# Optimization experiments

Hardware: AMD Instinct MI355X
Metric: run time of the kernel (lower is better)

The kernel has to match this reference:

```python
import jax, jax.numpy as jnp
import numpy as np

B, L, D, H, DH = 1, 256, 128, 4, 32  # batch, seq, d_pair, n_head, d_hidden


def setup_inputs() -> dict:
    key = jax.random.key(0)
    ks = jax.random.split(key, 8)
    s = 0.02  # init scale for weights
    return {
        "pair": jax.random.normal(ks[0], (B, L, L, D), jnp.float32),
        "ln_w": jnp.ones((D,), jnp.float32),
        "ln_b": jnp.zeros((D,), jnp.float32),
        "Wq": jax.random.normal(ks[1], (D, H * DH), jnp.float32) * s,
        "Wk": jax.random.normal(ks[2], (D, H * DH), jnp.float32) * s,
        "Wv": jax.random.normal(ks[3], (D, H * DH), jnp.float32) * s,
        "Wb": jax.random.normal(ks[4], (D, H), jnp.float32) * s,
        "Wg": jax.random.normal(ks[5], (D, H * DH), jnp.float32) * s,
        "bg": jnp.ones((H * DH,), jnp.float32),
        "Wo": jax.random.normal(ks[6], (H * DH, D), jnp.float32) * s,
        "bo": jnp.zeros((D,), jnp.float32),
    }


def reference(pair, ln_w, ln_b, Wq, Wk, Wv, Wb, Wg, bg, Wo, bo):
    scale = DH ** -0.5
    # LayerNorm over d_pair
    mu = jnp.mean(pair, axis=-1, keepdims=True)
    var = jnp.mean((pair - mu) ** 2, axis=-1, keepdims=True)
    x = (pair - mu) * jax.lax.rsqrt(var + 1e-5) * ln_w + ln_b
    b, l = x.shape[0], x.shape[1]
    bias = jnp.einsum('bijd,dh->bijh', x, Wb)            # (B, L, L, H)
    gate = jax.nn.sigmoid(x @ Wg + bg)                   # (B, L, L, H*DH)
    q = (x @ Wq).reshape(b, l, l, H, DH) * scale
    k = (x @ Wk).reshape(b, l, l, H, DH)
    v = (x @ Wv).reshape(b, l, l, H, DH)
    # triangle attention over k (third L axis), bias shared across i
    attn = jnp.einsum('bijhd,bikhd->bijkh', q, k) + bias[:, None]
    attn = jax.nn.softmax(attn, axis=3)
    out = jnp.einsum('bijkh,bikhd->bijhd', attn, v).reshape(b, l, l, H * DH)
    out = gate * out
    return out @ Wo + bo
```

## Files before the change

kernel.cpp:

```cpp
#include <hip/hip_runtime.h>
#include <math.h>

#define NPOS 65536

typedef _Float16 f16x8 __attribute__((ext_vector_type(8)));
typedef _Float16 f16x4 __attribute__((ext_vector_type(4)));
typedef float    f32x4 __attribute__((ext_vector_type(4)));

__device__ __forceinline__ unsigned short f16bits(_Float16 h) {
    return __builtin_bit_cast(unsigned short, h);
}

__global__ __launch_bounds__(256) void split_w_kernel(
    const float* __restrict__ Wq, const float* __restrict__ Wk,
    const float* __restrict__ Wv, const float* __restrict__ Wg,
    const float* __restrict__ Wo,
    _Float16* __restrict__ Wt_hi, _Float16* __restrict__ WoT_hi)
{
    int t = blockIdx.x * 256 + threadIdx.x;
    if (t < 65536) {
        int ng = t >> 7, kk = t & 127;
        int mat = ng >> 7, n = ng & 127;
        const float* W = (mat == 0) ? Wq : (mat == 1) ? Wk : (mat == 2) ? Wv : Wg;
        Wt_hi[t] = (_Float16)W[kk * 128 + n];
    } else {
        int tt = t - 65536;
        int n = tt >> 7, kk = tt & 127;
        WoT_hi[tt] = (_Float16)Wo[kk * 128 + n];
    }
}

__global__ __launch_bounds__(256, 4) void ln_proj_kernel(
    const float* __restrict__ pair, const float* __restrict__ ln_w, const float* __restrict__ ln_b,
    const float* __restrict__ Wb, const float* __restrict__ bg,
    const _Float16* __restrict__ Wt_hi,
    _Float16* __restrict__ q_hi, _Float16* __restrict__ q_lo,
    _Float16* __restrict__ k16, _Float16* __restrict__ v16, _Float16* __restrict__ g16,
    float* __restrict__ bias_n)
{
    __shared__ _Float16 xbuf[2][64][136];
    _Float16 (*xh)[136] = xbuf[0];
    _Float16 (*xl)[136] = xbuf[1];

    const int tid = threadIdx.x;
    const int p0  = blockIdx.x * 64;
    const int r   = tid >> 2;
    const int cb  = (tid & 3) * 32;

    float xv[32];
    {
        const float4* pr = (const float4*)(pair + (size_t)(p0 + r) * 128 + cb);
        #pragma unroll
        for (int i = 0; i < 8; ++i) {
            float4 t = pr[i];
            xv[i * 4 + 0] = t.x; xv[i * 4 + 1] = t.y;
            xv[i * 4 + 2] = t.z; xv[i * 4 + 3] = t.w;
        }
    }
    float sum = 0.f, sq = 0.f;
    #pragma unroll
    for (int i = 0; i < 32; ++i) { sum += xv[i]; sq += xv[i] * xv[i]; }
    sum += __shfl_xor(sum, 1); sq += __shfl_xor(sq, 1);
    sum += __shfl_xor(sum, 2); sq += __shfl_xor(sq, 2);
    float mean = sum * (1.f / 128.f);
    float var  = sq * (1.f / 128.f) - mean * mean;
    float rstd = rsqrtf(var + 1e-5f);

    float b0 = 0.f, b1 = 0.f, b2 = 0.f, b3 = 0.f;
    #pragma unroll
    for (int i8 = 0; i8 < 4; ++i8) {
        float4 lw0 = *(const float4*)(ln_w + cb + i8 * 8);
        float4 lw1 = *(const float4*)(ln_w + cb + i8 * 8 + 4);
        float4 lb0 = *(const float4*)(ln_b + cb + i8 * 8);
        float4 lb1 = *(const float4*)(ln_b + cb + i8 * 8 + 4);
        float lw[8] = {lw0.x, lw0.y, lw0.z, lw0.w, lw1.x, lw1.y, lw1.z, lw1.w};
        float lb[8] = {lb0.x, lb0.y, lb0.z, lb0.w, lb1.x, lb1.y, lb1.z, lb1.w};
        f16x8 hv, lv;
        #pragma unroll
        for (int j = 0; j < 8; ++j) {
            int i = i8 * 8 + j;
            float xn = (xv[i] - mean) * rstd * lw[j] + lb[j];
            _Float16 h = (_Float16)xn;
            hv[j] = h;
            lv[j] = (_Float16)((xn - (float)h) * 2048.0f);
            float4 wb = *(const float4*)(Wb + (size_t)(cb + i) * 4);
            b0 = fmaf(xn, wb.x, b0); b1 = fmaf(xn, wb.y, b1);
            b2 = fmaf(xn, wb.z, b2); b3 = fmaf(xn, wb.w, b3);
        }
        *(f16x8*)&xh[r][cb + i8 * 8] = hv;
        *(f16x8*)&xl[r][cb + i8 * 8] = lv;
    }
    b0 += __shfl_xor(b0, 1); b1 += __shfl_xor(b1, 1);
    b2 += __shfl_xor(b2, 1); b3 += __shfl_xor(b3, 1);
    b0 += __shfl_xor(b0, 2); b1 += __shfl_xor(b1, 2);
    b2 += __shfl_xor(b2, 2); b3 += __shfl_xor(b3, 2);
    if ((tid & 3) == 0) {
        int p = p0 + r;
        bias_n[0 * NPOS + p] = b0;
        bias_n[1 * NPOS + p] = b1;
        bias_n[2 * NPOS + p] = b2;
        bias_n[3 * NPOS + p] = b3;
    }
    __syncthreads();

    const int w  = tid >> 6, l = tid & 63;
    const int lm = l & 15, lg = l >> 4;
    const int arow = w * 16 + lm;

    f16x8 ahf[4], alf[4];
    #pragma unroll
    for (int kt = 0; kt < 4; ++kt) {
        ahf[kt] = *(const f16x8*)&xh[arow][kt * 32 + lg * 8];
        alf[kt] = *(const f16x8*)&xl[arow][kt * 32 + lg * 8];
    }

    _Float16 (*Bh)[136] = xbuf[0];
    unsigned* stg = (unsigned*)&xbuf[1][0][0];

    const float scale = 0.17677669529663687f;

    for (int chunk = 0; chunk < 8; ++chunk) {
        __syncthreads();

        const _Float16* srch = Wt_hi + (size_t)(chunk * 64) * 128;
        f16x8 breg[4];
        #pragma unroll
        for (int it = 0; it < 4; ++it) {
            int idx = it * 256 + tid;
            breg[it] = *(const f16x8*)(srch + (idx >> 4) * 128 + (idx & 15) * 8);
        }

        if (chunk > 0) {
            const int pm = (chunk - 1) >> 1, pcol = ((chunk - 1) & 1) * 64;
            #pragma unroll
            for (int it = 0; it < 4; ++it) {
                int idx = it * 256 + tid;
                int row = idx >> 4, c4 = (idx & 15) * 4;
                uint4 pk = *(const uint4*)&stg[row * 68 + c4];
                ushort4 hv = make_ushort4((unsigned short)(pk.x & 0xffff),
                                          (unsigned short)(pk.y & 0xffff),
                                          (unsigned short)(pk.z & 0xffff),
                                          (unsigned short)(pk.w & 0xffff));
                size_t off = (size_t)(p0 + row) * 128 + pcol + c4;
                if (pm == 0) {
                    *(ushort4*)(q_hi + off) = hv;
                    ushort4 lv = make_ushort4((unsigned short)(pk.x >> 16),
                                              (unsigned short)(pk.y >> 16),
                                              (unsigned short)(pk.z >> 16),
                                              (unsigned short)(pk.w >> 16));
                    *(ushort4*)(q_lo + off) = lv;
                } else if (pm == 1) *(ushort4*)(k16 + off) = hv;
                else if   (pm == 2) *(ushort4*)(v16 + off) = hv;
                else                *(ushort4*)(g16 + off) = hv;
            }
        }

        #pragma unroll
        for (int it = 0; it < 4; ++it) {
            int idx = it * 256 + tid;
            *(f16x8*)&Bh[idx >> 4][(idx & 15) * 8] = breg[it];
        }
        __syncthreads();

        const int mat = chunk >> 1;
        f32x4 acch[4], accc[4];
        #pragma unroll
        for (int ct = 0; ct < 4; ++ct) {
            acch[ct] = (f32x4){0.f, 0.f, 0.f, 0.f};
            accc[ct] = (f32x4){0.f, 0.f, 0.f, 0.f};
        }
        #pragma unroll
        for (int kt = 0; kt < 4; ++kt) {
            const int koff = kt * 32 + lg * 8;
            #pragma unroll
            for (int ct = 0; ct < 4; ++ct) {
                f16x8 bh = *(const f16x8*)&Bh[ct * 16 + lm][koff];
                acch[ct] = __builtin_amdgcn_mfma_f32_16x16x32_f16(ahf[kt], bh, acch[ct], 0, 0, 0);
                accc[ct] = __builtin_amdgcn_mfma_f32_16x16x32_f16(alf[kt], bh, accc[ct], 0, 0, 0);
            }
        }

        const int colhalf = (chunk & 1) * 64;
        #pragma unroll
        for (int ct = 0; ct < 4; ++ct) {
            const int col = ct * 16 + lm;
            float bgv = (mat == 3) ? bg[colhalf + col] : 0.f;
            #pragma unroll
            for (int rr = 0; rr < 4; ++rr) {
                float val = acch[ct][rr] + accc[ct][rr] * (1.0f / 2048.0f);
                if (mat == 0) val *= scale;
                if (mat == 3) val = 1.f / (1.f + __expf(-(val + bgv)));
                _Float16 h = (_Float16)val;
                unsigned pk = f16bits(h);
                if (mat == 0) {
                    _Float16 lo = (_Float16)((val - (float)h) * 2048.0f);
                    pk |= ((unsigned)f16bits(lo)) << 16;
                }
                stg[(w * 16 + lg * 4 + rr) * 68 + col] = pk;
            }
        }
    }

    __syncthreads();
    {
        #pragma unroll
        for (int it = 0; it < 4; ++it) {
            int idx = it * 256 + tid;
            int row = idx >> 4, c4 = (idx & 15) * 4;
            uint4 pk = *(const uint4*)&stg[row * 68 + c4];
            ushort4 hv = make_ushort4((unsigned short)(pk.x & 0xffff),
                                      (unsigned short)(pk.y & 0xffff),
                                      (unsigned short)(pk.z & 0xffff),
                                      (unsigned short)(pk.w & 0xffff));
            *(ushort4*)(g16 + (size_t)(p0 + row) * 128 + 64 + c4) = hv;
        }
    }
}

__global__ __launch_bounds__(256, 3) void attn_kernel(
    const _Float16* __restrict__ q_hi, const _Float16* __restrict__ q_lo,
    const _Float16* __restrict__ k16, const _Float16* __restrict__ v16,
    const _Float16* __restrict__ g16, const float* __restrict__ bias_n,
    float* __restrict__ go)
{
    __shared__ _Float16 Khs[64][44];
    __shared__ _Float16 Vts[32][76];
    __shared__ _Float16 Pb[4][32][76];

    const int tid  = threadIdx.x;
    const int w    = tid >> 6;
    const int lane = tid & 63;
    const int lg   = lane >> 4, lm = lane & 15;
    const int i = blockIdx.x >> 2, h = blockIdx.x & 3;
    const size_t base = (size_t)i * 256 * 128 + (size_t)h * 32;
    const int j0w = w * 64;

    f16x8 qh[4], ql[4];
    #pragma unroll
    for (int jt = 0; jt < 4; ++jt) {
        size_t off = base + (size_t)(j0w + jt * 16 + lm) * 128 + lg * 8;
        qh[jt] = *(const f16x8*)(q_hi + off);
        ql[jt] = *(const f16x8*)(q_lo + off);
    }

    float Oacc[2][4][4] = {};
    float mrow[4], lrow[4];
    #pragma unroll
    for (int jt = 0; jt < 4; ++jt) { mrow[jt] = -1e30f; lrow[jt] = 0.f; }

    const int sr  = tid >> 2;
    const int sc8 = (tid & 3) * 8;

    f16x8 kpre = *(const f16x8*)(k16 + base + (size_t)sr * 128 + sc8);
    f16x8 vpre = *(const f16x8*)(v16 + base + (size_t)sr * 128 + sc8);

    for (int kc = 0; kc < 256; kc += 64) {
        __syncthreads();
        *(f16x8*)&Khs[sr][sc8] = kpre;
        #pragma unroll
        for (int e = 0; e < 8; ++e) Vts[sc8 + e][sr] = vpre[e];
        __syncthreads();
        if (kc + 64 < 256) {
            kpre = *(const f16x8*)(k16 + base + (size_t)(kc + 64 + sr) * 128 + sc8);
            vpre = *(const f16x8*)(v16 + base + (size_t)(kc + 64 + sr) * 128 + sc8);
        }

        f16x8 kf[4];
        #pragma unroll
        for (int t = 0; t < 4; ++t) kf[t] = *(const f16x8*)&Khs[t * 16 + lm][lg * 8];
        f16x8 vf[2][2];
        #pragma unroll
        for (int dt = 0; dt < 2; ++dt)
            #pragma unroll
            for (int ks = 0; ks < 2; ++ks)
                vf[dt][ks] = *(const f16x8*)&Vts[dt * 16 + lm][ks * 32 + lg * 8];

        #pragma unroll
        for (int jh2 = 0; jh2 < 2; ++jh2) {
            #pragma unroll
            for (int t2 = 0; t2 < 2; ++t2) {
                const int jt = jh2 * 2 + t2;
                const float* bj = bias_n + (size_t)h * NPOS
                                + (size_t)(j0w + jt * 16 + lm) * 256 + kc + lg * 4;
                float s[16];
                #pragma unroll
                for (int t = 0; t < 4; ++t) {
                    float4 bv = *(const float4*)(bj + t * 16);
                    f32x4 c  = {bv.x, bv.y, bv.z, bv.w};
                    f32x4 cl = {0.f, 0.f, 0.f, 0.f};
                    c  = __builtin_amdgcn_mfma_f32_16x16x32_f16(kf[t], qh[jt], c,  0, 0, 0);
                    cl = __builtin_amdgcn_mfma_f32_16x16x32_f16(kf[t], ql[jt], cl, 0, 0, 0);
                    #pragma unroll
                    for (int rr = 0; rr < 4; ++rr)
                        s[t * 4 + rr] = c[rr] + cl[rr] * (1.0f / 2048.0f);
                }
                float mx = s[0];
                #pragma unroll
                for (int e = 1; e < 16; ++e) mx = fmaxf(mx, s[e]);
                mx = fmaxf(mx, __shfl_xor(mx, 16));
                mx = fmaxf(mx, __shfl_xor(mx, 32));
                float mn = fmaxf(mrow[jt], mx);
                float alpha = __expf(mrow[jt] - mn);
                mrow[jt] = mn;
                float ps = 0.f;
                #pragma unroll
                for (int e = 0; e < 16; ++e) { s[e] = __expf(s[e] - mn); ps += s[e]; }
                ps += __shfl_xor(ps, 16);
                ps += __shfl_xor(ps, 32);
                lrow[jt] = lrow[jt] * alpha + ps;
                #pragma unroll
                for (int dt = 0; dt < 2; ++dt)
                    #pragma unroll
                    for (int rr = 0; rr < 4; ++rr) Oacc[dt][jt][rr] *= alpha;
                #pragma unroll
                for (int t = 0; t < 4; ++t) {
                    f16x4 pv;
                    #pragma unroll
                    for (int rr = 0; rr < 4; ++rr) pv[rr] = (_Float16)s[t * 4 + rr];
                    *(f16x4*)&Pb[w][t2 * 16 + lm][t * 16 + lg * 4] = pv;
                }
            }

            #pragma unroll
            for (int t2 = 0; t2 < 2; ++t2) {
                const int jt = jh2 * 2 + t2;
                f16x8 pf0 = *(const f16x8*)&Pb[w][t2 * 16 + lm][lg * 8];
                f16x8 pf1 = *(const f16x8*)&Pb[w][t2 * 16 + lm][32 + lg * 8];
                #pragma unroll
                for (int dt = 0; dt < 2; ++dt) {
                    f32x4 c = {Oacc[dt][jt][0], Oacc[dt][jt][1], Oacc[dt][jt][2], Oacc[dt][jt][3]};
                    c = __builtin_amdgcn_mfma_f32_16x16x32_f16(vf[dt][0], pf0, c, 0, 0, 0);
                    c = __builtin_amdgcn_mfma_f32_16x16x32_f16(vf[dt][1], pf1, c, 0, 0, 0);
                    Oacc[dt][jt][0] = c[0]; Oacc[dt][jt][1] = c[1];
                    Oacc[dt][jt][2] = c[2]; Oacc[dt][jt][3] = c[3];
                }
            }
        }
    }

    #pragma unroll
    for (int jt = 0; jt < 4; ++jt) {
        const int j = j0w + jt * 16 + lm;
        const float inv = 1.0f / lrow[jt];
        #pragma unroll
        for (int dt = 0; dt < 2; ++dt) {
            f16x4 gv4 = *(const f16x4*)(g16 + base + (size_t)j * 128 + dt * 16 + lg * 4);
            float4 ov;
            ov.x = Oacc[dt][jt][0] * inv * (float)gv4[0];
            ov.y = Oacc[dt][jt][1] * inv * (float)gv4[1];
            ov.z = Oacc[dt][jt][2] * inv * (float)gv4[2];
            ov.w = Oacc[dt][jt][3] * inv * (float)gv4[3];
            *(float4*)(go + base + (size_t)j * 128 + dt * 16 + lg * 4) = ov;
        }
    }
}

__global__ __launch_bounds__(256, 3) void out_proj_kernel(
    const float* __restrict__ go, const _Float16* __restrict__ WoT_hi,
    const float* __restrict__ bo, float* __restrict__ out)
{
    __shared__ _Float16 xh[64][136];
    __shared__ _Float16 xl[64][136];
    __shared__ _Float16 Bh[64][136];

    const int tid = threadIdx.x;
    const int p0  = blockIdx.x * 64;
    const int r   = tid >> 2;
    const int cb  = (tid & 3) * 32;

    {
        const float4* pr = (const float4*)(go + (size_t)(p0 + r) * 128 + cb);
        #pragma unroll
        for (int i8 = 0; i8 < 4; ++i8) {
            float4 a = pr[i8 * 2], b = pr[i8 * 2 + 1];
            float v[8] = {a.x, a.y, a.z, a.w, b.x, b.y, b.z, b.w};
            f16x8 hv, lv;
            #pragma unroll
            for (int j = 0; j < 8; ++j) {
                _Float16 h = (_Float16)v[j];
                hv[j] = h;
                lv[j] = (_Float16)((v[j] - (float)h) * 2048.0f);
            }
            *(f16x8*)&xh[r][cb + i8 * 8] = hv;
            *(f16x8*)&xl[r][cb + i8 * 8] = lv;
        }
    }
    __syncthreads();

    const int w  = tid >> 6, l = tid & 63;
    const int lm = l & 15, lg = l >> 4;
    const int arow = w * 16 + lm;

    f16x8 ahf[4], alf[4];
    #pragma unroll
    for (int kt = 0; kt < 4; ++kt) {
        ahf[kt] = *(const f16x8*)&xh[arow][kt * 32 + lg * 8];
        alf[kt] = *(const f16x8*)&xl[arow][kt * 32 + lg * 8];
    }

    #pragma unroll
    for (int chunk = 0; chunk < 2; ++chunk) {
        const _Float16* srch = WoT_hi + (size_t)(chunk * 64) * 128;
        f16x8 breg[4];
        #pragma unroll
        for (int it = 0; it < 4; ++it) {
            int idx = it * 256 + tid;
            breg[it] = *(const f16x8*)(srch + (idx >> 4) * 128 + (idx & 15) * 8);
        }
        if (chunk > 0) __syncthreads();
        #pragma unroll
        for (int it = 0; it < 4; ++it) {
            int idx = it * 256 + tid;
            *(f16x8*)&Bh[idx >> 4][(idx & 15) * 8] = breg[it];
        }
        __syncthreads();

        f32x4 acch[4], accc[4];
        #pragma unroll
        for (int ct = 0; ct < 4; ++ct) {
            acch[ct] = (f32x4){0.f, 0.f, 0.f, 0.f};
            accc[ct] = (f32x4){0.f, 0.f, 0.f, 0.f};
        }
        #pragma unroll
        for (int kt = 0; kt < 4; ++kt) {
            const int koff = kt * 32 + lg * 8;
            #pragma unroll
            for (int ct = 0; ct < 4; ++ct) {
                f16x8 bh = *(const f16x8*)&Bh[ct * 16 + lm][koff];
                acch[ct] = __builtin_amdgcn_mfma_f32_16x16x32_f16(ahf[kt], bh, acch[ct], 0, 0, 0);
                accc[ct] = __builtin_amdgcn_mfma_f32_16x16x32_f16(alf[kt], bh, accc[ct], 0, 0, 0);
            }
        }

        #pragma unroll
        for (int ct = 0; ct < 4; ++ct) {
            const int col = chunk * 64 + ct * 16 + lm;
            const float bov = bo[col];
            #pragma unroll
            for (int rr = 0; rr < 4; ++rr) {
                const int row = p0 + w * 16 + lg * 4 + rr;
                out[(size_t)row * 128 + col] =
                    acch[ct][rr] + accc[ct][rr] * (1.0f / 2048.0f) + bov;
            }
        }
    }
}

extern "C" void kernel_launch(void* const* d_in, const int* in_sizes, int n_in,
                              void* d_out, int out_size, void* d_ws, size_t ws_size,
                              hipStream_t stream) {
    const float* pair = (const float*)d_in[0];
    const float* ln_w = (const float*)d_in[1];
    const float* ln_b = (const float*)d_in[2];
    const float* Wq   = (const float*)d_in[3];
    const float* Wk   = (const float*)d_in[4];
    const float* Wv   = (const float*)d_in[5];
    const float* Wb   = (const float*)d_in[6];
    const float* Wg   = (const float*)d_in[7];
    const float* bg   = (const float*)d_in[8];
    const float* Wo   = (const float*)d_in[9];
    const float* bo   = (const float*)d_in[10];

    _Float16* q_hi = (_Float16*)d_ws;
    _Float16* q_lo = q_hi + (size_t)NPOS * 128;
    _Float16* k16  = q_lo + (size_t)NPOS * 128;
    _Float16* v16  = k16 + (size_t)NPOS * 128;
    _Float16* g16  = v16 + (size_t)NPOS * 128;
    float* go      = (float*)(g16 + (size_t)NPOS * 128);
    float* bias_n  = go + (size_t)NPOS * 128;
    _Float16* WoT_hi = (_Float16*)(bias_n + 4 * (size_t)NPOS);
    float* out     = (float*)d_out;

    _Float16* Wt_hi = (_Float16*)d_out;

    hipLaunchKernelGGL(split_w_kernel, dim3(320), dim3(256), 0, stream,
                       Wq, Wk, Wv, Wg, Wo, Wt_hi, WoT_hi);
    hipLaunchKernelGGL(ln_proj_kernel, dim3(1024), dim3(256), 0, stream,
                       pair, ln_w, ln_b, Wb, bg, Wt_hi,
                       q_hi, q_lo, k16, v16, g16, bias_n);
    hipLaunchKernelGGL(attn_kernel, dim3(1024), dim3(256), 0, stream,
                       q_hi, q_lo, k16, v16, g16, bias_n, go);
    hipLaunchKernelGGL(out_proj_kernel, dim3(1024), dim3(256), 0, stream,
                       go, WoT_hi, bo, out);
}
```

Baseline: 248.3 us.

## Split attention into single-wave blocks, one per 64-row j chunk

The attention kernel now launches 4096 blocks of 64 threads, each a single wavefront covering 64 query rows for one (i, h), instead of 1024 blocks of four waves. Because each block is one wave, the __syncthreads barriers go away. The register prefetch of K/V is replaced by direct loads into shared memory, and the P buffer shrinks to one 16-row tile. The trade-off is that each wave now loads K/V for its own (i, h), so that traffic is four times higher, and with no prefetch the global load latency is exposed in every chunk.

Measured after the change: 275.7 us. +11.0%, slower.

```diff
diff --git a/kernel.cpp b/kernel.cpp
--- a/kernel.cpp
+++ b/kernel.cpp
@@ -217,7 +217,7 @@
     }
 }
 
-__global__ __launch_bounds__(256, 3) void attn_kernel(
+__global__ __launch_bounds__(64, 3) void attn_kernel(
     const _Float16* __restrict__ q_hi, const _Float16* __restrict__ q_lo,
     const _Float16* __restrict__ k16, const _Float16* __restrict__ v16,
     const _Float16* __restrict__ g16, const float* __restrict__ bias_n,
@@ -225,15 +225,16 @@
 {
     __shared__ _Float16 Khs[64][44];
     __shared__ _Float16 Vts[32][76];
-    __shared__ _Float16 Pb[4][32][76];
-
-    const int tid  = threadIdx.x;
-    const int w    = tid >> 6;
-    const int lane = tid & 63;
+    __shared__ _Float16 Pb[16][76];
+
+    const int lane = threadIdx.x;
     const int lg   = lane >> 4, lm = lane & 15;
-    const int i = blockIdx.x >> 2, h = blockIdx.x & 3;
+    const int bid  = blockIdx.x;
+    const int i    = bid >> 4;
+    const int h    = (bid >> 2) & 3;
+    const int jq   = bid & 3;
     const size_t base = (size_t)i * 256 * 128 + (size_t)h * 32;
-    const int j0w = w * 64;
+    const int j0w = jq * 64;
 
     f16x8 qh[4], ql[4];
     #pragma unroll
@@ -248,21 +249,16 @@
     #pragma unroll
     for (int jt = 0; jt < 4; ++jt) { mrow[jt] = -1e30f; lrow[jt] = 0.f; }
 
-    const int sr  = tid >> 2;
-    const int sc8 = (tid & 3) * 8;
-
-    f16x8 kpre = *(const f16x8*)(k16 + base + (size_t)sr * 128 + sc8);
-    f16x8 vpre = *(const f16x8*)(v16 + base + (size_t)sr * 128 + sc8);
-
     for (int kc = 0; kc < 256; kc += 64) {
-        __syncthreads();
-        *(f16x8*)&Khs[sr][sc8] = kpre;
-        #pragma unroll
-        for (int e = 0; e < 8; ++e) Vts[sc8 + e][sr] = vpre[e];
-        __syncthreads();
-        if (kc + 64 < 256) {
-            kpre = *(const f16x8*)(k16 + base + (size_t)(kc + 64 + sr) * 128 + sc8);
-            vpre = *(const f16x8*)(v16 + base + (size_t)(kc + 64 + sr) * 128 + sc8);
+        #pragma unroll
+        for (int it = 0; it < 4; ++it) {
+            int idx = it * 64 + lane;
+            int sr = idx >> 2, sc8 = (idx & 3) * 8;
+            f16x8 kv = *(const f16x8*)(k16 + base + (size_t)(kc + sr) * 128 + sc8);
+            f16x8 vv = *(const f16x8*)(v16 + base + (size_t)(kc + sr) * 128 + sc8);
+            *(f16x8*)&Khs[sr][sc8] = kv;
+            #pragma unroll
+            for (int e = 0; e < 8; ++e) Vts[sc8 + e][sr] = vv[e];
         }
 
         f16x8 kf[4];
@@ -276,64 +272,56 @@
                 vf[dt][ks] = *(const f16x8*)&Vts[dt * 16 + lm][ks * 32 + lg * 8];
 
         #pragma unroll
-        for (int jh2 = 0; jh2 < 2; ++jh2) {
-            #pragma unroll
-            for (int t2 = 0; t2 < 2; ++t2) {
-                const int jt = jh2 * 2 + t2;
-                const float* bj = bias_n + (size_t)h * NPOS
-                                + (size_t)(j0w + jt * 16 + lm) * 256 + kc + lg * 4;
-                float s[16];
+        for (int jt = 0; jt < 4; ++jt) {
+            const float* bj = bias_n + (size_t)h * NPOS
+                            + (size_t)(j0w + jt * 16 + lm) * 256 + kc + lg * 4;
+            float s[16];
+            #pragma unroll
+            for (int t = 0; t < 4; ++t) {
+                float4 bv = *(const float4*)(bj + t * 16);
+                f32x4 c  = {bv.x, bv.y, bv.z, bv.w};
+                f32x4 cl = {0.f, 0.f, 0.f, 0.f};
+                c  = __builtin_amdgcn_mfma_f32_16x16x32_f16(kf[t], qh[jt], c,  0, 0, 0);
+                cl = __builtin_amdgcn_mfma_f32_16x16x32_f16(kf[t], ql[jt], cl, 0, 0, 0);
                 #pragma unroll
-                for (int t = 0; t < 4; ++t) {
-                    float4 bv = *(const float4*)(bj + t * 16);
-                    f32x4 c  = {bv.x, bv.y, bv.z, bv.w};
-                    f32x4 cl = {0.f, 0.f, 0.f, 0.f};
-                    c  = __builtin_amdgcn_mfma_f32_16x16x32_f16(kf[t], qh[jt], c,  0, 0, 0);
-                    cl = __builtin_amdgcn_mfma_f32_16x16x32_f16(kf[t], ql[jt], cl, 0, 0, 0);
-                    #pragma unroll
-                    for (int rr = 0; rr < 4; ++rr)
-                        s[t * 4 + rr] = c[rr] + cl[rr] * (1.0f / 2048.0f);
-                }
-                float mx = s[0];
+                for (int rr = 0; rr < 4; ++rr)
+                    s[t * 4 + rr] = c[rr] + cl[rr] * (1.0f / 2048.0f);
+            }
+            float mx = s[0];
+            #pragma unroll
+            for (int e = 1; e < 16; ++e) mx = fmaxf(mx, s[e]);
+            mx = fmaxf(mx, __shfl_xor(mx, 16));
+            mx = fmaxf(mx, __shfl_xor(mx, 32));
+            float mn = fmaxf(mrow[jt], mx);
+            float alpha = __expf(mrow[jt] - mn);
+            mrow[jt] = mn;
+            float ps = 0.f;
+            #pragma unroll
+            for (int e = 0; e < 16; ++e) { s[e] = __expf(s[e] - mn); ps += s[e]; }
+            ps += __shfl_xor(ps, 16);
+            ps += __shfl_xor(ps, 32);
+            lrow[jt] = lrow[jt] * alpha + ps;
+            #pragma unroll
+            for (int dt = 0; dt < 2; ++dt)
                 #pragma unroll
-                for (int e = 1; e < 16; ++e) mx = fmaxf(mx, s[e]);
-                mx = fmaxf(mx, __shfl_xor(mx, 16));
-                mx = fmaxf(mx, __shfl_xor(mx, 32));
-                float mn = fmaxf(mrow[jt], mx);
-                float alpha = __expf(mrow[jt] - mn);
-                mrow[jt] = mn;
-                float ps = 0.f;
+                for (int rr = 0; rr < 4; ++rr) Oacc[dt][jt][rr] *= alpha;
+
+            #pragma unroll
+            for (int t = 0; t < 4; ++t) {
+                f16x4 pv;
                 #pragma unroll
-                for (int e = 0; e < 16; ++e) { s[e] = __expf(s[e] - mn); ps += s[e]; }
-                ps += __shfl_xor(ps, 16);
-                ps += __shfl_xor(ps, 32);
-                lrow[jt] = lrow[jt] * alpha + ps;
-                #pragma unroll
-                for (int dt = 0; dt < 2; ++dt)
-                    #pragma unroll
-                    for (int rr = 0; rr < 4; ++rr) Oacc[dt][jt][rr] *= alpha;
-                #pragma unroll
-                for (int t = 0; t < 4; ++t) {
-                    f16x4 pv;
-                    #pragma unroll
-                    for (int rr = 0; rr < 4; ++rr) pv[rr] = (_Float16)s[t * 4 + rr];
-                    *(f16x4*)&Pb[w][t2 * 16 + lm][t * 16 + lg * 4] = pv;
-                }
-            }
-
-            #pragma unroll
-            for (int t2 = 0; t2 < 2; ++t2) {
-                const int jt = jh2 * 2 + t2;
-                f16x8 pf0 = *(const f16x8*)&Pb[w][t2 * 16 + lm][lg * 8];
-                f16x8 pf1 = *(const f16x8*)&Pb[w][t2 * 16 + lm][32 + lg * 8];
-                #pragma unroll
-                for (int dt = 0; dt < 2; ++dt) {
-                    f32x4 c = {Oacc[dt][jt][0], Oacc[dt][jt][1], Oacc[dt][jt][2], Oacc[dt][jt][3]};
-                    c = __builtin_amdgcn_mfma_f32_16x16x32_f16(vf[dt][0], pf0, c, 0, 0, 0);
-                    c = __builtin_amdgcn_mfma_f32_16x16x32_f16(vf[dt][1], pf1, c, 0, 0, 0);
-                    Oacc[dt][jt][0] = c[0]; Oacc[dt][jt][1] = c[1];
-                    Oacc[dt][jt][2] = c[2]; Oacc[dt][jt][3] = c[3];
-                }
+                for (int rr = 0; rr < 4; ++rr) pv[rr] = (_Float16)s[t * 4 + rr];
+                *(f16x4*)&Pb[lm][t * 16 + lg * 4] = pv;
+            }
+            f16x8 pf0 = *(const f16x8*)&Pb[lm][lg * 8];
+            f16x8 pf1 = *(const f16x8*)&Pb[lm][32 + lg * 8];
+            #pragma unroll
+            for (int dt = 0; dt < 2; ++dt) {
+                f32x4 c = {Oacc[dt][jt][0], Oacc[dt][jt][1], Oacc[dt][jt][2], Oacc[dt][jt][3]};
+                c = __builtin_amdgcn_mfma_f32_16x16x32_f16(vf[dt][0], pf0, c, 0, 0, 0);
+                c = __builtin_amdgcn_mfma_f32_16x16x32_f16(vf[dt][1], pf1, c, 0, 0, 0);
+                Oacc[dt][jt][0] = c[0]; Oacc[dt][jt][1] = c[1];
+                Oacc[dt][jt][2] = c[2]; Oacc[dt][jt][3] = c[3];
             }
         }
     }
@@ -478,7 +466,7 @@
     hipLaunchKernelGGL(ln_proj_kernel, dim3(1024), dim3(256), 0, stream,
                        pair, ln_w, ln_b, Wb, bg, Wt_hi,
                        q_hi, q_lo, k16, v16, g16, bias_n);
-    hipLaunchKernelGGL(attn_kernel, dim3(1024), dim3(256), 0, stream,
+    hipLaunchKernelGGL(attn_kernel, dim3(4096), dim3(64), 0, stream,
                        q_hi, q_lo, k16, v16, g16, bias_n, go);
     hipLaunchKernelGGL(out_proj_kernel, dim3(1024), dim3(256), 0, stream,
                        go, WoT_hi, bo, out);
```

## Double-buffer K/V tiles in LDS and hoist bias loads ahead of MFMA

Applied to the files above, without the earlier changes.

Double-buffers the K and V shared-memory tiles so the next chunk is written into the alternate buffer after compute, which removes one of the two barriers per chunk. The four bias float4 loads for each row tile are now issued up front and added after the MFMAs, rather than being fed in as the accumulator input. This gives the loads more time to land before use. In exchange, LDS use grows by about 8.6KB per block, which could lower occupancy under launch_bounds(256,3), and the scores also cost 16 extra adds.

Result: slower. 399.3 us (+60.8%).

```diff
diff --git a/kernel.cpp b/kernel.cpp
--- a/kernel.cpp
+++ b/kernel.cpp
@@ -223,8 +223,8 @@
     const _Float16* __restrict__ g16, const float* __restrict__ bias_n,
     float* __restrict__ go)
 {
-    __shared__ _Float16 Khs[64][44];
-    __shared__ _Float16 Vts[32][76];
+    __shared__ _Float16 Khs[2][64][44];
+    __shared__ _Float16 Vts[2][32][76];
     __shared__ _Float16 Pb[4][32][76];
 
     const int tid  = threadIdx.x;
@@ -251,29 +251,34 @@
     const int sr  = tid >> 2;
     const int sc8 = (tid & 3) * 8;
 
-    f16x8 kpre = *(const f16x8*)(k16 + base + (size_t)sr * 128 + sc8);
-    f16x8 vpre = *(const f16x8*)(v16 + base + (size_t)sr * 128 + sc8);
-
-    for (int kc = 0; kc < 256; kc += 64) {
-        __syncthreads();
-        *(f16x8*)&Khs[sr][sc8] = kpre;
-        #pragma unroll
-        for (int e = 0; e < 8; ++e) Vts[sc8 + e][sr] = vpre[e];
-        __syncthreads();
-        if (kc + 64 < 256) {
+    {
+        f16x8 k0 = *(const f16x8*)(k16 + base + (size_t)sr * 128 + sc8);
+        f16x8 v0 = *(const f16x8*)(v16 + base + (size_t)sr * 128 + sc8);
+        *(f16x8*)&Khs[0][sr][sc8] = k0;
+        #pragma unroll
+        for (int e = 0; e < 8; ++e) Vts[0][sc8 + e][sr] = v0[e];
+    }
+    __syncthreads();
+
+    f16x8 kpre, vpre;
+    #pragma unroll
+    for (int p = 0; p < 4; ++p) {
+        const int cur = p & 1;
+        const int kc  = p * 64;
+        if (p < 3) {
             kpre = *(const f16x8*)(k16 + base + (size_t)(kc + 64 + sr) * 128 + sc8);
             vpre = *(const f16x8*)(v16 + base + (size_t)(kc + 64 + sr) * 128 + sc8);
         }
 
         f16x8 kf[4];
         #pragma unroll
-        for (int t = 0; t < 4; ++t) kf[t] = *(const f16x8*)&Khs[t * 16 + lm][lg * 8];
+        for (int t = 0; t < 4; ++t) kf[t] = *(const f16x8*)&Khs[cur][t * 16 + lm][lg * 8];
         f16x8 vf[2][2];
         #pragma unroll
         for (int dt = 0; dt < 2; ++dt)
             #pragma unroll
             for (int ks = 0; ks < 2; ++ks)
-                vf[dt][ks] = *(const f16x8*)&Vts[dt * 16 + lm][ks * 32 + lg * 8];
+                vf[dt][ks] = *(const f16x8*)&Vts[cur][dt * 16 + lm][ks * 32 + lg * 8];
 
         #pragma unroll
         for (int jh2 = 0; jh2 < 2; ++jh2) {
@@ -282,11 +287,14 @@
                 const int jt = jh2 * 2 + t2;
                 const float* bj = bias_n + (size_t)h * NPOS
                                 + (size_t)(j0w + jt * 16 + lm) * 256 + kc + lg * 4;
+                float4 bv0 = *(const float4*)(bj);
+                float4 bv1 = *(const float4*)(bj + 16);
+                float4 bv2 = *(const float4*)(bj + 32);
+                float4 bv3 = *(const float4*)(bj + 48);
                 float s[16];
                 #pragma unroll
                 for (int t = 0; t < 4; ++t) {
-                    float4 bv = *(const float4*)(bj + t * 16);
-                    f32x4 c  = {bv.x, bv.y, bv.z, bv.w};
+                    f32x4 c  = {0.f, 0.f, 0.f, 0.f};
                     f32x4 cl = {0.f, 0.f, 0.f, 0.f};
                     c  = __builtin_amdgcn_mfma_f32_16x16x32_f16(kf[t], qh[jt], c,  0, 0, 0);
                     cl = __builtin_amdgcn_mfma_f32_16x16x32_f16(kf[t], ql[jt], cl, 0, 0, 0);
@@ -294,6 +302,10 @@
                     for (int rr = 0; rr < 4; ++rr)
                         s[t * 4 + rr] = c[rr] + cl[rr] * (1.0f / 2048.0f);
                 }
+                s[0]  += bv0.x; s[1]  += bv0.y; s[2]  += bv0.z; s[3]  += bv0.w;
+                s[4]  += bv1.x; s[5]  += bv1.y; s[6]  += bv1.z; s[7]  += bv1.w;
+                s[8]  += bv2.x; s[9]  += bv2.y; s[10] += bv2.z; s[11] += bv2.w;
+                s[12] += bv3.x; s[13] += bv3.y; s[14] += bv3.z; s[15] += bv3.w;
                 float mx = s[0];
                 #pragma unroll
                 for (int e = 1; e < 16; ++e) mx = fmaxf(mx, s[e]);
@@ -336,6 +348,13 @@
                 }
             }
         }
+
+        if (p < 3) {
+            *(f16x8*)&Khs[cur ^ 1][sr][sc8] = kpre;
+            #pragma unroll
+            for (int e = 0; e < 8; ++e) Vts[cur ^ 1][sc8 + e][sr] = vpre[e];
+            __syncthreads();
+        }
     }
 
     #pragma unroll
```
